# Optimization experiments

Hardware: AMD Instinct MI355X
Metric: run time of the kernel (lower is better)

The kernel has to match this reference:

```python
import jax, jax.numpy as jnp
import numpy as np

N = 50000      # nodes
E = 800000     # edges (avg degree 16)
IN = 256       # in_feats
H = 128        # hidden_feats
C = 40         # out_feats == num classes (label dim)
LPA_ITERS = 10


def setup_inputs() -> dict:
    key = jax.random.key(0)
    ks = jax.random.split(key, 9)
    features = jax.random.normal(ks[0], (N, IN), dtype=jnp.float32)
    labels = jax.random.normal(ks[1], (N, C), dtype=jnp.float32)
    mask = jax.random.randint(ks[2], (N,), 0, 2) > 0          # bool [N]
    src = jax.random.randint(ks[3], (E,), 0, N, dtype=jnp.int32)
    dst = jax.random.randint(ks[4], (E,), 0, N, dtype=jnp.int32)
    W1 = jax.random.normal(ks[5], (IN, H), dtype=jnp.float32) * (1.0 / np.sqrt(IN))
    b1 = jnp.zeros((H,), dtype=jnp.float32)
    W2 = jax.random.normal(ks[6], (H, C), dtype=jnp.float32) * (1.0 / np.sqrt(H))
    b2 = jnp.zeros((C,), dtype=jnp.float32)
    return {"features": features, "labels": labels, "mask": mask,
            "src": src, "dst": dst, "W1": W1, "b1": b1, "W2": W2, "b2": b2}


def reference(features, labels, mask, src, dst, W1, b1, W2, b2):
    ones_e = jnp.ones((E,), dtype=jnp.float32)
    deg_out = jax.ops.segment_sum(ones_e, src, num_segments=N)  # out-degree
    deg_in = jax.ops.segment_sum(ones_e, dst, num_segments=N)   # in-degree
    norm_src = jnp.maximum(deg_out, 1.0) ** -0.5                 # DGL clamps deg>=1
    norm_dst = jnp.maximum(deg_in, 1.0) ** -0.5

    def gconv(x, W, b):
        # DGL GraphConv, norm='both': D_in^{-1/2} A^T D_out^{-1/2} (x W) + b
        h = (x @ W) * norm_src[:, None]                          # [N, d_out]
        agg = jax.ops.segment_sum(h[src], dst, num_segments=N)   # gather+scatter-add
        return agg * norm_dst[:, None] + b

    x = jax.nn.relu(gconv(features, W1, b1))
    # dropout identity in eval mode
    x = gconv(x, W2, b2)

    # Label propagation: adj[src,dst]=1 so (adj @ y)[i] = sum_{(i->j)} y[j]
    masked_labels = jnp.where(mask[:, None], labels, 0.0)

    def step(y, _):
        y = jax.ops.segment_sum(y[dst], src, num_segments=N)
        y = jnp.where(mask[:, None], labels, y)
        return y, None

    y, _ = jax.lax.scan(step, masked_labels, None, length=LPA_ITERS)
    return x, y
```

## Files before the change

### kernel.cpp

```cpp
#include <hip/hip_runtime.h>

#define Nn 50000
#define Ee 800000
#define INF_ 256
#define HID 128
#define NC 40
#define CAPD 48
#define CAPS 48
#define LPA_ITERS 10
#define NB 98
#define BSH 9
#define EPB 1024
#define NBLK ((Ee + EPB - 1) / EPB)
#define G1_ROWS 64
#define G1BLK ((Nn + G1_ROWS - 1) / G1_ROWS)
#define CAPB_D 10240
#define CAPB_S 6144
#define AGG1_BLKS 2500
#define LPA_BLKS ((Nn + 31) / 32)
#define GEMM2_BLKS ((Nn + 319) / 320)
#define SCB 196

typedef __attribute__((ext_vector_type(8))) short bfrag;
typedef __attribute__((ext_vector_type(4))) float ffrag;

__device__ inline unsigned f2bf2(float a, float b) {
    unsigned ua = __float_as_uint(a); ua += 0x7FFFu + ((ua >> 16) & 1u);
    unsigned ub = __float_as_uint(b); ub += 0x7FFFu + ((ub >> 16) & 1u);
    return (ua >> 16) | (ub & 0xFFFF0000u);
}
__device__ inline unsigned short f2bf(float a) {
    unsigned ua = __float_as_uint(a); ua += 0x7FFFu + ((ua >> 16) & 1u);
    return (unsigned short)(ua >> 16);
}
__device__ inline float bf_lo(unsigned u) { return __uint_as_float(u << 16); }
__device__ inline float bf_hi(unsigned u) { return __uint_as_float(u & 0xFFFF0000u); }

__device__ inline bool read_mask(const void* mask, int node, int fmt) {
    if (fmt) return ((const unsigned char*)mask)[node] != 0;
    return ((const int*)mask)[node] != 0;
}

__global__ __launch_bounds__(256) void detect_prep(
    const unsigned int* __restrict__ m, int* flag,
    const float* __restrict__ W1, unsigned short* __restrict__ W1t) {
    int bb = blockIdx.x, tid = threadIdx.x;
    if (bb < 49) {
        int i = bb * 256 + tid;
        if (i < 12500) {
            if (m[i] > 1u) atomicOr(flag, 1);
        }
    } else {
        int c = bb - 49;
        W1t[c * INF_ + tid] = f2bf(W1[(size_t)tid * HID + c]);
    }
}

__global__ __launch_bounds__(256) void phase1(
    const int* __restrict__ src, const int* __restrict__ dst,
    const void* __restrict__ mask, const int* __restrict__ flag,
    int* __restrict__ cnt_src, int* __restrict__ cur_d, int* __restrict__ cur_s,
    unsigned* __restrict__ bkt_d, unsigned* __restrict__ bkt_s,
    const float* __restrict__ feat, const unsigned short* __restrict__ W1t,
    unsigned short* __restrict__ h1b) {
    __shared__ uint4 smem[784];
    const int tid = threadIdx.x;
    if (blockIdx.x < NBLK) {
        unsigned* stage_d = (unsigned*)smem;
        unsigned* stage_s = stage_d + EPB;
        int* hd  = (int*)(stage_s + EPB);
        int* od  = hd + NB;
        int* cd  = od + NB + 1;
        int* gd_ = cd + NB;
        int* hs  = gd_ + NB;
        int* os_ = hs + NB;
        int* cs_ = os_ + NB + 1;
        int* gs_ = cs_ + NB;
        int lane = tid & 63;
        int wid = tid >> 6;
        int e0 = blockIdx.x * EPB;
        int fmt = *flag;
        if (tid < NB) { hd[tid] = 0; hs[tid] = 0; }
        __syncthreads();

        int rs[EPB / 256], rd[EPB / 256];
        unsigned um = 0;
#pragma unroll
        for (int k = 0; k < EPB / 256; k++) {
            int e = e0 + tid + k * 256;
            rs[k] = -1; rd[k] = -1;
            if (e < Ee) {
                int s = src[e], d = dst[e];
                rs[k] = s; rd[k] = d;
                atomicAdd(&cnt_src[s], 1);
                atomicAdd(&hd[d >> BSH], 1);
                if (!read_mask(mask, s, fmt)) {
                    um |= (1u << k);
                    atomicAdd(&hs[s >> BSH], 1);
                }
            }
        }
        __syncthreads();
        if (wid < 2) {
            int* h = wid ? hs : hd;
            int* o = wid ? os_ : od;
            int i0 = lane * 2;
            int v0 = (i0 < NB) ? h[i0] : 0;
            int v1 = (i0 + 1 < NB) ? h[i0 + 1] : 0;
            int s = v0 + v1;
#pragma unroll
            for (int d = 1; d < 64; d <<= 1) {
                int t = __shfl_up(s, d);
                if (lane >= d) s += t;
            }
            int excl = s - v0 - v1;
            if (i0 < NB) o[i0] = excl;
            if (i0 + 1 < NB) o[i0 + 1] = excl + v0;
            if (lane == 63) o[NB] = s;
        }
        __syncthreads();
        if (tid < NB) {
            gd_[tid] = hd[tid] ? atomicAdd(&cur_d[tid], hd[tid]) : 0;
            gs_[tid] = hs[tid] ? atomicAdd(&cur_s[tid], hs[tid]) : 0;
            cd[tid] = od[tid];
            cs_[tid] = os_[tid];
        }
        __syncthreads();
#pragma unroll
        for (int k = 0; k < EPB / 256; k++) {
            if (rd[k] >= 0) {
                int p = atomicAdd(&cd[rd[k] >> BSH], 1);
                stage_d[p] = ((unsigned)rd[k] << 16) | (unsigned)rs[k];
                if (um & (1u << k)) {
                    int q = atomicAdd(&cs_[rs[k] >> BSH], 1);
                    stage_s[q] = ((unsigned)rs[k] << 16) | (unsigned)rd[k];
                }
            }
        }
        __syncthreads();
        for (int b = wid; b < NB; b += 4) {
            int base = od[b], cntb = hd[b], g0 = gd_[b];
            unsigned* gb = bkt_d + (size_t)b * CAPB_D;
            for (int i = lane; i < cntb; i += 64) {
                int pos = g0 + i;
                if (pos < CAPB_D) gb[pos] = stage_d[base + i];
            }
            int bs = os_[b], cnts = hs[b], gs0 = gs_[b];
            unsigned* gbs = bkt_s + (size_t)b * CAPB_S;
            for (int i = lane; i < cnts; i += 64) {
                int pos = gs0 + i;
                if (pos < CAPB_S) gbs[pos] = stage_s[bs + i];
            }
        }
    } else {
        unsigned short* lA = (unsigned short*)smem;
        unsigned short* lB = lA + G1_ROWS * 32;
        const int row0 = (blockIdx.x - NBLK) * G1_ROWS;
        const int w = tid >> 6;
        const int l = tid & 63;
        const int lane15 = l & 15;
        const int quad = l >> 4;
        const int rw0 = w * 16;

        ffrag acc[8];
#pragma unroll
        for (int t = 0; t < 8; t++) acc[t] = (ffrag){0.f, 0.f, 0.f, 0.f};

        for (int k0 = 0; k0 < INF_; k0 += 32) {
#pragma unroll
            for (int p = 0; p < 2; p++) {
                int idx = tid + p * 256;
                int r = idx >> 3, c4 = idx & 7;
                int grow = row0 + r;
                float4 v = make_float4(0.f, 0.f, 0.f, 0.f);
                if (grow < Nn)
                    v = *(const float4*)(feat + (size_t)grow * INF_ + k0 + c4 * 4);
                uint2 pk;
                pk.x = f2bf2(v.x, v.y);
                pk.y = f2bf2(v.z, v.w);
                *(uint2*)((char*)lA + r * 64 + c4 * 8) = pk;
            }
#pragma unroll
            for (int p = 0; p < 2; p++) {
                int idx = tid + p * 256;
                int col = idx >> 2, q = idx & 3;
                uint4 v = *(const uint4*)((const char*)W1t + col * 512 + k0 * 2 + q * 16);
                *(uint4*)((char*)lB + col * 64 + q * 16) = v;
            }
            __syncthreads();
            int arow = rw0 + lane15;
            bfrag af = *(const bfrag*)((const char*)lA + arow * 64 + quad * 16);
#pragma unroll
            for (int t = 0; t < 8; t++) {
                int col = t * 16 + lane15;
                bfrag bf = *(const bfrag*)((const char*)lB + col * 64 + quad * 16);
                acc[t] = __builtin_amdgcn_mfma_f32_16x16x32_bf16(af, bf, acc[t], 0, 0, 0);
            }
            __syncthreads();
        }
#pragma unroll
        for (int t = 0; t < 8; t++) {
#pragma unroll
            for (int i = 0; i < 4; i++) {
                int grow = row0 + rw0 + quad * 4 + i;
                if (grow < Nn)
                    h1b[(size_t)grow * HID + t * 16 + lane15] = f2bf(acc[t][i]);
            }
        }
    }
}

__global__ __launch_bounds__(256) void build_csr_both(
    const unsigned* __restrict__ bkt_d, const int* __restrict__ cur_d,
    const unsigned* __restrict__ bkt_s, const int* __restrict__ cur_s,
    const void* __restrict__ mask, const int* __restrict__ flag,
    const int* __restrict__ cnt_src,
    int* __restrict__ adj_dst, int* __restrict__ cnt_dst,
    int* __restrict__ adj_s, int* __restrict__ cnt_u, int* __restrict__ cnt_m,
    int* __restrict__ n_un, int* __restrict__ ulist,
    unsigned short* __restrict__ h1b) {
    __shared__ int lu[512], lm[512];
    int bb = blockIdx.x, tid = threadIdx.x;
    lu[tid] = 0; lu[tid + 256] = 0; lm[tid] = 0; lm[tid + 256] = 0;
    __syncthreads();
    if (bb < NB) {
        int b = bb;
        int n = cur_d[b]; if (n > CAPB_D) n = CAPB_D;
        int n0 = b << BSH;
        const unsigned* base = bkt_d + (size_t)b * CAPB_D;
        for (int i = tid; i < n; i += 256) {
            unsigned r = base[i];
            int d = r >> 16, s = r & 0xffff;
            int sl = atomicAdd(&lu[d - n0], 1);
            if (sl < CAPD) adj_dst[d * CAPD + sl] = s;
        }
        __syncthreads();
        int g0 = n0 + tid;
        if (g0 < Nn) cnt_dst[g0] = lu[tid];
        g0 += 256;
        if (g0 < Nn) cnt_dst[g0] = lu[tid + 256];
    } else if (bb < 2 * NB) {
        int b = bb - NB;
        int fmt = *flag;
        int n = cur_s[b]; if (n > CAPB_S) n = CAPB_S;
        int n0 = b << BSH;
        const unsigned* base = bkt_s + (size_t)b * CAPB_S;
        for (int i = tid; i < n; i += 256) {
            unsigned r = base[i];
            int s = r >> 16, d = r & 0xffff;
            if (read_mask(mask, d, fmt)) {
                int sl = atomicAdd(&lm[s - n0], 1);
                if (sl < CAPS) adj_s[s * CAPS + (CAPS - 1 - sl)] = d;
            } else {
                int sl = atomicAdd(&lu[s - n0], 1);
                if (sl < CAPS) adj_s[s * CAPS + sl] = d;
            }
        }
        __syncthreads();
        int g0 = n0 + tid;
        if (g0 < Nn) {
            cnt_u[g0] = lu[tid]; cnt_m[g0] = lm[tid];
            if (!read_mask(mask, g0, fmt)) {
                int p = atomicAdd(n_un, 1);
                ulist[p] = g0;
            }
        }
        g0 += 256;
        if (g0 < Nn) {
            cnt_u[g0] = lu[tid + 256]; cnt_m[g0] = lm[tid + 256];
            if (!read_mask(mask, g0, fmt)) {
                int p = atomicAdd(n_un, 1);
                ulist[p] = g0;
            }
        }
    } else {
        int b = bb - 2 * NB;
        int rbase = b * 256;
        int c8 = tid & 7;
#pragma unroll 1
        for (int it = 0; it < 8; it++) {
            int r = rbase + it * 32 + (tid >> 3);
            if (r >= Nn) continue;
            int cs = cnt_src[r];
            float nr = rsqrtf((float)(cs > 1 ? cs : 1));
            uint4* row = (uint4*)(h1b + (size_t)r * HID);
#pragma unroll
            for (int h = 0; h < 2; h++) {
                uint4 u = row[c8 * 2 + h];
                u.x = f2bf2(bf_lo(u.x) * nr, bf_hi(u.x) * nr);
                u.y = f2bf2(bf_lo(u.y) * nr, bf_hi(u.y) * nr);
                u.z = f2bf2(bf_lo(u.z) * nr, bf_hi(u.z) * nr);
                u.w = f2bf2(bf_lo(u.w) * nr, bf_hi(u.w) * nr);
                row[c8 * 2 + h] = u;
            }
        }
    }
}


__device__ inline void do_lpa_const(
    int g, int l, const float4* __restrict__ labels,
    const int* __restrict__ ulist, const int* __restrict__ adj_s,
    const int* __restrict__ cnt_m, float4* __restrict__ sconst,
    uint2* __restrict__ y1b) {
    int u = ulist[g];
    int cm = cnt_m[u];
    int cnt = cm < CAPS ? cm : CAPS;
    const int* lst = adj_s + (size_t)u * CAPS + (CAPS - cnt);
    float4 s = make_float4(0.f, 0.f, 0.f, 0.f);
    int e = 0;
    for (; e + 8 <= cnt; e += 8) {
        float4 v[8];
#pragma unroll
        for (int q = 0; q < 8; q++) v[q] = labels[(size_t)lst[e + q] * 10 + l];
#pragma unroll
        for (int q = 0; q < 8; q++) {
            s.x += v[q].x; s.y += v[q].y; s.z += v[q].z; s.w += v[q].w;
        }
    }
    for (; e + 4 <= cnt; e += 4) {
        float4 v[4];
#pragma unroll
        for (int q = 0; q < 4; q++) v[q] = labels[(size_t)lst[e + q] * 10 + l];
#pragma unroll
        for (int q = 0; q < 4; q++) {
            s.x += v[q].x; s.y += v[q].y; s.z += v[q].z; s.w += v[q].w;
        }
    }
    for (; e < cnt; e++) {
        float4 a = labels[(size_t)lst[e] * 10 + l];
        s.x += a.x; s.y += a.y; s.z += a.z; s.w += a.w;
    }
    sconst[(size_t)u * 10 + l] = s;
    uint2 pk; pk.x = f2bf2(s.x, s.y); pk.y = f2bf2(s.z, s.w);
    y1b[(size_t)u * 10 + l] = pk;
}

__device__ inline void do_lpa_mid(
    int g, int l, const uint2* __restrict__ ycur,
    const int* __restrict__ ulist, const int* __restrict__ adj_s,
    const int* __restrict__ cnt_u, const float4* __restrict__ sconst,
    uint2* __restrict__ ynext) {
    int u = ulist[g];
    int cu = cnt_u[u];
    int cnt = cu < CAPS ? cu : CAPS;
    const int* lst = adj_s + (size_t)u * CAPS;
    float4 s = sconst[(size_t)u * 10 + l];
    int e = 0;
    for (; e + 8 <= cnt; e += 8) {
        uint2 v[8];
#pragma unroll
        for (int q = 0; q < 8; q++) v[q] = ycur[(size_t)lst[e + q] * 10 + l];
#pragma unroll
        for (int q = 0; q < 8; q++) {
            s.x += bf_lo(v[q].x); s.y += bf_hi(v[q].x);
            s.z += bf_lo(v[q].y); s.w += bf_hi(v[q].y);
        }
    }
    for (; e + 4 <= cnt; e += 4) {
        uint2 v[4];
#pragma unroll
        for (int q = 0; q < 4; q++) v[q] = ycur[(size_t)lst[e + q] * 10 + l];
#pragma unroll
        for (int q = 0; q < 4; q++) {
            s.x += bf_lo(v[q].x); s.y += bf_hi(v[q].x);
            s.z += bf_lo(v[q].y); s.w += bf_hi(v[q].y);
        }
    }
    for (; e < cnt; e++) {
        uint2 v = ycur[(size_t)lst[e] * 10 + l];
        s.x += bf_lo(v.x); s.y += bf_hi(v.x);
        s.z += bf_lo(v.y); s.w += bf_hi(v.y);
    }
    uint2 pk; pk.x = f2bf2(s.x, s.y); pk.y = f2bf2(s.z, s.w);
    ynext[(size_t)u * 10 + l] = pk;
}

__device__ inline void do_agg2(
    int node, int l, const uint2* __restrict__ h2b,
    const int* __restrict__ adj_dst, const int* __restrict__ cnt_dst,
    const float4* __restrict__ b2, float4* __restrict__ out_x) {
    int dg = cnt_dst[node];
    int cnt = dg < CAPD ? dg : CAPD;
    const int* lst = adj_dst + (size_t)node * CAPD;
    float s0 = 0.f, s1 = 0.f, s2 = 0.f, s3 = 0.f;
    int e = 0;
    for (; e + 8 <= cnt; e += 8) {
        uint2 u[8];
#pragma unroll
        for (int q = 0; q < 8; q++) u[q] = h2b[(size_t)lst[e + q] * 10 + l];
#pragma unroll
        for (int q = 0; q < 8; q++) {
            s0 += bf_lo(u[q].x); s1 += bf_hi(u[q].x);
            s2 += bf_lo(u[q].y); s3 += bf_hi(u[q].y);
        }
    }
    for (; e + 4 <= cnt; e += 4) {
        uint2 u[4];
#pragma unroll
        for (int q = 0; q < 4; q++) u[q] = h2b[(size_t)lst[e + q] * 10 + l];
#pragma unroll
        for (int q = 0; q < 4; q++) {
            s0 += bf_lo(u[q].x); s1 += bf_hi(u[q].x);
            s2 += bf_lo(u[q].y); s3 += bf_hi(u[q].y);
        }
    }
    for (; e < cnt; e++) {
        uint2 u = h2b[(size_t)lst[e] * 10 + l];
        s0 += bf_lo(u.x); s1 += bf_hi(u.x);
        s2 += bf_lo(u.y); s3 += bf_hi(u.y);
    }
    float nrm = rsqrtf((float)(dg > 1 ? dg : 1));
    float4 bb = b2[l];
    float4 v;
    v.x = s0 * nrm + bb.x;
    v.y = s1 * nrm + bb.y;
    v.z = s2 * nrm + bb.z;
    v.w = s3 * nrm + bb.w;
    out_x[(size_t)node * 10 + l] = v;
}

__global__ __launch_bounds__(320) void k_agg1_lconst(
    const uint4* __restrict__ h1b, const int* __restrict__ adj_dst,
    const int* __restrict__ cnt_dst, const float4* __restrict__ b1,
    uint4* __restrict__ x1b,
    const float4* __restrict__ labels, const void* __restrict__ mask,
    const int* __restrict__ flag, const int* __restrict__ n_un,
    const int* __restrict__ ulist, const int* __restrict__ adj_s,
    const int* __restrict__ cnt_m, float4* __restrict__ sconst,
    uint2* __restrict__ y1b, float4* __restrict__ out_y4) {
    int bb = blockIdx.x, tid = threadIdx.x;
    if (bb < AGG1_BLKS) {
        const int node = bb * 20 + (tid >> 4);
        const int l = tid & 15;
        int dg = cnt_dst[node];
        int cnt = dg < CAPD ? dg : CAPD;
        const int* lst = adj_dst + (size_t)node * CAPD;
        float s0 = 0.f, s1 = 0.f, s2 = 0.f, s3 = 0.f;
        float s4 = 0.f, s5 = 0.f, s6 = 0.f, s7 = 0.f;
        int e = 0;
        for (; e + 8 <= cnt; e += 8) {
            uint4 u[8];
#pragma unroll
            for (int q = 0; q < 8; q++) u[q] = h1b[(size_t)lst[e + q] * 16 + l];
#pragma unroll
            for (int q = 0; q < 8; q++) {
                s0 += bf_lo(u[q].x); s1 += bf_hi(u[q].x);
                s2 += bf_lo(u[q].y); s3 += bf_hi(u[q].y);
                s4 += bf_lo(u[q].z); s5 += bf_hi(u[q].z);
                s6 += bf_lo(u[q].w); s7 += bf_hi(u[q].w);
            }
        }
        for (; e < cnt; e++) {
            uint4 u = h1b[(size_t)lst[e] * 16 + l];
            s0 += bf_lo(u.x); s1 += bf_hi(u.x);
            s2 += bf_lo(u.y); s3 += bf_hi(u.y);
            s4 += bf_lo(u.z); s5 += bf_hi(u.z);
            s6 += bf_lo(u.w); s7 += bf_hi(u.w);
        }
        float nrm = rsqrtf((float)(dg > 1 ? dg : 1));
        float4 bb0 = b1[l * 2], bb1 = b1[l * 2 + 1];
        float v0x = fmaxf(s0 * nrm + bb0.x, 0.f);
        float v0y = fmaxf(s1 * nrm + bb0.y, 0.f);
        float v0z = fmaxf(s2 * nrm + bb0.z, 0.f);
        float v0w = fmaxf(s3 * nrm + bb0.w, 0.f);
        float v1x = fmaxf(s4 * nrm + bb1.x, 0.f);
        float v1y = fmaxf(s5 * nrm + bb1.y, 0.f);
        float v1z = fmaxf(s6 * nrm + bb1.z, 0.f);
        float v1w = fmaxf(s7 * nrm + bb1.w, 0.f);
        uint4 pk4;
        pk4.x = f2bf2(v0x, v0y);
        pk4.y = f2bf2(v0z, v0w);
        pk4.z = f2bf2(v1x, v1y);
        pk4.w = f2bf2(v1z, v1w);
        x1b[(size_t)node * 16 + l] = pk4;
    } else {
        int lb = bb - AGG1_BLKS;
        int fmt = *flag;
        int i = lb * 320 + tid;
        if (i < Nn * 10) {
            int node = i / 10;
            if (read_mask(mask, node, fmt)) out_y4[i] = labels[i];
        }
        int g = lb * 32 + tid / 10;
        if (g < *n_un)
            do_lpa_const(g, tid % 10, labels, ulist, adj_s, cnt_m, sconst, y1b);
    }
}

__global__ __launch_bounds__(320) void k_gemm2_mid(
    const uint4* __restrict__ x1b, const float4* __restrict__ W2,
    const int* __restrict__ cnt_src, unsigned* __restrict__ h2b,
    const uint2* __restrict__ ycur, const int* __restrict__ n_un,
    const int* __restrict__ ulist, const int* __restrict__ adj_s,
    const int* __restrict__ cnt_u, const float4* __restrict__ sconst,
    uint2* __restrict__ ynext) {
    __shared__ float lw[HID * NC];
    int bb = blockIdx.x, tid = threadIdx.x;
    if (bb < GEMM2_BLKS) {
        for (int i = tid; i < HID * NC / 4; i += 320)
            ((float4*)lw)[i] = W2[i];
        __syncthreads();
        int r = bb * 320 + tid;
        if (r >= Nn) return;
        const uint4* xr = x1b + (size_t)r * 16;
        float4 acc[10];
#pragma unroll
        for (int j = 0; j < 10; j++) acc[j] = make_float4(0.f, 0.f, 0.f, 0.f);
        for (int kk = 0; kk < 16; kk++) {
            uint4 u = xr[kk];
            float xv[8];
            xv[0] = bf_lo(u.x); xv[1] = bf_hi(u.x);
            xv[2] = bf_lo(u.y); xv[3] = bf_hi(u.y);
            xv[4] = bf_lo(u.z); xv[5] = bf_hi(u.z);
            xv[6] = bf_lo(u.w); xv[7] = bf_hi(u.w);
#pragma unroll
            for (int s = 0; s < 8; s++) {
                float x = xv[s];
                const float4* wrow = (const float4*)(lw + (kk * 8 + s) * NC);
#pragma unroll
                for (int j = 0; j < 10; j++) {
                    float4 w = wrow[j];
                    acc[j].x += x * w.x; acc[j].y += x * w.y;
                    acc[j].z += x * w.z; acc[j].w += x * w.w;
                }
            }
        }
        int dg = cnt_src[r];
        float nrm = rsqrtf((float)(dg > 1 ? dg : 1));
        uint2* out = (uint2*)(h2b + (size_t)r * 20);
#pragma unroll
        for (int j = 0; j < 10; j++) {
            uint2 pk;
            pk.x = f2bf2(acc[j].x * nrm, acc[j].y * nrm);
            pk.y = f2bf2(acc[j].z * nrm, acc[j].w * nrm);
            out[j] = pk;
        }
    } else {
        int g = (bb - GEMM2_BLKS) * 32 + tid / 10;
        if (g < *n_un)
            do_lpa_mid(g, tid % 10, ycur, ulist, adj_s, cnt_u, sconst, ynext);
    }
}

__global__ __launch_bounds__(320) void k_agg2_mid(
    const uint2* __restrict__ h2b, const int* __restrict__ adj_dst,
    const int* __restrict__ cnt_dst, const float4* __restrict__ b2,
    float4* __restrict__ out_x,
    const uint2* __restrict__ ycur, const int* __restrict__ n_un,
    const int* __restrict__ ulist, const int* __restrict__ adj_s,
    const int* __restrict__ cnt_u, const float4* __restrict__ sconst,
    uint2* __restrict__ ynext) {
    int bb = blockIdx.x, tid = threadIdx.x;
    if (bb < LPA_BLKS) {
        int node = bb * 32 + tid / 10;
        if (node < Nn)
            do_agg2(node, tid % 10, h2b, adj_dst, cnt_dst, b2, out_x);
    } else {
        int g = (bb - LPA_BLKS) * 32 + tid / 10;
        if (g < *n_un)
            do_lpa_mid(g, tid % 10, ycur, ulist, adj_s, cnt_u, sconst, ynext);
    }
}

__global__ __launch_bounds__(320) void lpa_mid(
    const uint2* __restrict__ ycur, const int* __restrict__ n_un,
    const int* __restrict__ ulist, const int* __restrict__ adj_s,
    const int* __restrict__ cnt_u, const float4* __restrict__ sconst,
    uint2* __restrict__ ynext) {
    int g = blockIdx.x * 32 + threadIdx.x / 10;
    if (g < *n_un)
        do_lpa_mid(g, threadIdx.x % 10, ycur, ulist, adj_s, cnt_u, sconst, ynext);
}

__global__ __launch_bounds__(320) void lpa_last(
    const uint2* __restrict__ ycur, const int* __restrict__ n_un,
    const int* __restrict__ ulist, const int* __restrict__ adj_s,
    const int* __restrict__ cnt_u, const float4* __restrict__ sconst,
    float4* __restrict__ out_y) {
    int g = blockIdx.x * 32 + threadIdx.x / 10;
    int l = threadIdx.x % 10;
    if (g >= *n_un) return;
    int u = ulist[g];
    int cu = cnt_u[u];
    int cnt = cu < CAPS ? cu : CAPS;
    const int* lst = adj_s + (size_t)u * CAPS;
    float4 s = sconst[(size_t)u * 10 + l];
    int e = 0;
    for (; e + 8 <= cnt; e += 8) {
        uint2 v[8];
#pragma unroll
        for (int q = 0; q < 8; q++) v[q] = ycur[(size_t)lst[e + q] * 10 + l];
#pragma unroll
        for (int q = 0; q < 8; q++) {
            s.x += bf_lo(v[q].x); s.y += bf_hi(v[q].x);
            s.z += bf_lo(v[q].y); s.w += bf_hi(v[q].y);
        }
    }
    for (; e + 4 <= cnt; e += 4) {
        uint2 v[4];
#pragma unroll
        for (int q = 0; q < 4; q++) v[q] = ycur[(size_t)lst[e + q] * 10 + l];
#pragma unroll
        for (int q = 0; q < 4; q++) {
            s.x += bf_lo(v[q].x); s.y += bf_hi(v[q].x);
            s.z += bf_lo(v[q].y); s.w += bf_hi(v[q].y);
        }
    }
    for (; e < cnt; e++) {
        uint2 v = ycur[(size_t)lst[e] * 10 + l];
        s.x += bf_lo(v.x); s.y += bf_hi(v.x);
        s.z += bf_lo(v.y); s.w += bf_hi(v.y);
    }
    out_y[(size_t)u * 10 + l] = s;
}

extern "C" void kernel_launch(void* const* d_in, const int* in_sizes, int n_in,
                              void* d_out, int out_size, void* d_ws, size_t ws_size,
                              hipStream_t stream) {
    const float* feat   = (const float*)d_in[0];
    const float* labels = (const float*)d_in[1];
    const void*  mask   = d_in[2];
    const int*   src    = (const int*)d_in[3];
    const int*   dst    = (const int*)d_in[4];
    const float* W1     = (const float*)d_in[5];
    const float* b1     = (const float*)d_in[6];
    const float* W2     = (const float*)d_in[7];
    const float* b2     = (const float*)d_in[8];

    float* out_x = (float*)d_out;
    float* out_y = out_x + (size_t)Nn * NC;

    char* ws = (char*)d_ws;
    size_t off = 0;
    auto alloc = [&](size_t bytes) -> void* {
        void* p = ws + off;
        off += (bytes + 255) & ~(size_t)255;
        return p;
    };
    int* flag    = (int*)alloc(256);
    int* n_un    = flag + 1;
    int* cnt_src = (int*)alloc((size_t)Nn * 4);
    int* cur_d   = (int*)alloc(512);
    int* cur_s   = (int*)alloc(512);
    size_t zero_bytes = off;
    int* cnt_dst = (int*)alloc((size_t)Nn * 4);
    int* cnt_u   = (int*)alloc((size_t)Nn * 4);
    int* cnt_m   = (int*)alloc((size_t)Nn * 4);
    int* ulist   = (int*)alloc((size_t)Nn * 4);
    unsigned short* W1t = (unsigned short*)alloc((size_t)HID * INF_ * 2);
    unsigned* bkt_d = (unsigned*)alloc((size_t)NB * CAPB_D * 4);
    unsigned* bkt_s = (unsigned*)alloc((size_t)NB * CAPB_S * 4);
    unsigned short* h1b = (unsigned short*)alloc((size_t)Nn * HID * 2);
    uint4* x1b = (uint4*)alloc((size_t)Nn * HID * 2);
    int* adj_s   = (int*)alloc((size_t)Nn * CAPS * 4);
    int* adj_dst = (int*)alloc((size_t)Nn * CAPD * 4);
    unsigned* h2b = (unsigned*)alloc((size_t)Nn * NC * 2);
    float* sconst = (float*)alloc((size_t)Nn * NC * 4);
    uint2* y1b = (uint2*)alloc((size_t)Nn * NC * 2);
    uint2* y2b = (uint2*)alloc((size_t)Nn * NC * 2);

    hipMemsetAsync(d_ws, 0, zero_bytes, stream);

    detect_prep<<<49 + HID, 256, 0, stream>>>((const unsigned int*)mask, flag,
                                              W1, W1t);
    phase1<<<NBLK + G1BLK, 256, 0, stream>>>(
        src, dst, mask, flag, cnt_src, cur_d, cur_s, bkt_d, bkt_s,
        feat, W1t, h1b);
    build_csr_both<<<NB * 2 + SCB, 256, 0, stream>>>(
        bkt_d, cur_d, bkt_s, cur_s, mask, flag, cnt_src,
        adj_dst, cnt_dst, adj_s, cnt_u, cnt_m, n_un, ulist, h1b);

    k_agg1_lconst<<<AGG1_BLKS + LPA_BLKS, 320, 0, stream>>>(
        (const uint4*)h1b, adj_dst, cnt_dst, (const float4*)b1, x1b,
        (const float4*)labels, mask, flag, n_un, ulist, adj_s,
        cnt_m, (float4*)sconst, y1b, (float4*)out_y);
    k_gemm2_mid<<<GEMM2_BLKS + LPA_BLKS, 320, 0, stream>>>(
        (const uint4*)x1b, (const float4*)W2, cnt_src, h2b,
        y1b, n_un, ulist, adj_s, cnt_u, (const float4*)sconst, y2b);
    k_agg2_mid<<<LPA_BLKS + LPA_BLKS, 320, 0, stream>>>(
        (const uint2*)h2b, adj_dst, cnt_dst, (const float4*)b2, (float4*)out_x,
        y2b, n_un, ulist, adj_s, cnt_u, (const float4*)sconst, y1b);

    const uint2* cur = y1b;
    for (int i = 0; i < 6; i++) {
        uint2* nxt = (i & 1) ? y1b : y2b;
        lpa_mid<<<LPA_BLKS, 320, 0, stream>>>(
            cur, n_un, ulist, adj_s, cnt_u, (const float4*)sconst, nxt);
        cur = nxt;
    }
    lpa_last<<<LPA_BLKS, 320, 0, stream>>>(
        cur, n_un, ulist, adj_s, cnt_u, (const float4*)sconst, (float4*)out_y);
}
```

Measured before the change: 362.7 us.

## Split GCN stages into chunks co-scheduled with more label-propagation iterations

Result: slower. 396.7 us (+9.4%).

```diff
diff --git a/kernel.cpp b/kernel.cpp
--- a/kernel.cpp
+++ b/kernel.cpp
@@ -16,10 +16,15 @@
 #define G1BLK ((Nn + G1_ROWS - 1) / G1_ROWS)
 #define CAPB_D 10240
 #define CAPB_S 6144
-#define AGG1_BLKS 2500
 #define LPA_BLKS ((Nn + 31) / 32)
-#define GEMM2_BLKS ((Nn + 319) / 320)
 #define SCB 196
+#define A1T1 834
+#define A1T2 833
+#define A1T3 833
+#define G2H1 79
+#define G2H2 78
+#define AG2H1 782
+#define AG2H2 781
 
 typedef __attribute__((ext_vector_type(8))) short bfrag;
 typedef __attribute__((ext_vector_type(4))) float ffrag;
@@ -298,6 +303,53 @@
 }
 
 
+__device__ inline void do_agg1b(
+    int node, int l, const uint4* __restrict__ h1b,
+    const int* __restrict__ adj_dst, const int* __restrict__ cnt_dst,
+    const float4* __restrict__ b1, uint4* __restrict__ x1b) {
+    int dg = cnt_dst[node];
+    int cnt = dg < CAPD ? dg : CAPD;
+    const int* lst = adj_dst + (size_t)node * CAPD;
+    float s0 = 0.f, s1 = 0.f, s2 = 0.f, s3 = 0.f;
+    float s4 = 0.f, s5 = 0.f, s6 = 0.f, s7 = 0.f;
+    int e = 0;
+    for (; e + 8 <= cnt; e += 8) {
+        uint4 u[8];
+#pragma unroll
+        for (int q = 0; q < 8; q++) u[q] = h1b[(size_t)lst[e + q] * 16 + l];
+#pragma unroll
+        for (int q = 0; q < 8; q++) {
+            s0 += bf_lo(u[q].x); s1 += bf_hi(u[q].x);
+            s2 += bf_lo(u[q].y); s3 += bf_hi(u[q].y);
+            s4 += bf_lo(u[q].z); s5 += bf_hi(u[q].z);
+            s6 += bf_lo(u[q].w); s7 += bf_hi(u[q].w);
+        }
+    }
+    for (; e < cnt; e++) {
+        uint4 u = h1b[(size_t)lst[e] * 16 + l];
+        s0 += bf_lo(u.x); s1 += bf_hi(u.x);
+        s2 += bf_lo(u.y); s3 += bf_hi(u.y);
+        s4 += bf_lo(u.z); s5 += bf_hi(u.z);
+        s6 += bf_lo(u.w); s7 += bf_hi(u.w);
+    }
+    float nrm = rsqrtf((float)(dg > 1 ? dg : 1));
+    float4 bb0 = b1[l * 2], bb1 = b1[l * 2 + 1];
+    float v0x = fmaxf(s0 * nrm + bb0.x, 0.f);
+    float v0y = fmaxf(s1 * nrm + bb0.y, 0.f);
+    float v0z = fmaxf(s2 * nrm + bb0.z, 0.f);
+    float v0w = fmaxf(s3 * nrm + bb0.w, 0.f);
+    float v1x = fmaxf(s4 * nrm + bb1.x, 0.f);
+    float v1y = fmaxf(s5 * nrm + bb1.y, 0.f);
+    float v1z = fmaxf(s6 * nrm + bb1.z, 0.f);
+    float v1w = fmaxf(s7 * nrm + bb1.w, 0.f);
+    uint4 pk4;
+    pk4.x = f2bf2(v0x, v0y);
+    pk4.y = f2bf2(v0z, v0w);
+    pk4.z = f2bf2(v1x, v1y);
+    pk4.w = f2bf2(v1z, v1w);
+    x1b[(size_t)node * 16 + l] = pk4;
+}
+
 __device__ inline void do_lpa_const(
     int g, int l, const float4* __restrict__ labels,
     const int* __restrict__ ulist, const int* __restrict__ adj_s,
@@ -420,7 +472,9 @@
     out_x[(size_t)node * 10 + l] = v;
 }
 
+
 __global__ __launch_bounds__(320) void k_agg1_lconst(
+    const int node0, const int nagg,
     const uint4* __restrict__ h1b, const int* __restrict__ adj_dst,
     const int* __restrict__ cnt_dst, const float4* __restrict__ b1,
     uint4* __restrict__ x1b,
@@ -430,52 +484,11 @@
     const int* __restrict__ cnt_m, float4* __restrict__ sconst,
     uint2* __restrict__ y1b, float4* __restrict__ out_y4) {
     int bb = blockIdx.x, tid = threadIdx.x;
-    if (bb < AGG1_BLKS) {
-        const int node = bb * 20 + (tid >> 4);
-        const int l = tid & 15;
-        int dg = cnt_dst[node];
-        int cnt = dg < CAPD ? dg : CAPD;
-        const int* lst = adj_dst + (size_t)node * CAPD;
-        float s0 = 0.f, s1 = 0.f, s2 = 0.f, s3 = 0.f;
-        float s4 = 0.f, s5 = 0.f, s6 = 0.f, s7 = 0.f;
-        int e = 0;
-        for (; e + 8 <= cnt; e += 8) {
-            uint4 u[8];
-#pragma unroll
-            for (int q = 0; q < 8; q++) u[q] = h1b[(size_t)lst[e + q] * 16 + l];
-#pragma unroll
-            for (int q = 0; q < 8; q++) {
-                s0 += bf_lo(u[q].x); s1 += bf_hi(u[q].x);
-                s2 += bf_lo(u[q].y); s3 += bf_hi(u[q].y);
-                s4 += bf_lo(u[q].z); s5 += bf_hi(u[q].z);
-                s6 += bf_lo(u[q].w); s7 += bf_hi(u[q].w);
-            }
-        }
-        for (; e < cnt; e++) {
-            uint4 u = h1b[(size_t)lst[e] * 16 + l];
-            s0 += bf_lo(u.x); s1 += bf_hi(u.x);
-            s2 += bf_lo(u.y); s3 += bf_hi(u.y);
-            s4 += bf_lo(u.z); s5 += bf_hi(u.z);
-            s6 += bf_lo(u.w); s7 += bf_hi(u.w);
-        }
-        float nrm = rsqrtf((float)(dg > 1 ? dg : 1));
-        float4 bb0 = b1[l * 2], bb1 = b1[l * 2 + 1];
-        float v0x = fmaxf(s0 * nrm + bb0.x, 0.f);
-        float v0y = fmaxf(s1 * nrm + bb0.y, 0.f);
-        float v0z = fmaxf(s2 * nrm + bb0.z, 0.f);
-        float v0w = fmaxf(s3 * nrm + bb0.w, 0.f);
-        float v1x = fmaxf(s4 * nrm + bb1.x, 0.f);
-        float v1y = fmaxf(s5 * nrm + bb1.y, 0.f);
-        float v1z = fmaxf(s6 * nrm + bb1.z, 0.f);
-        float v1w = fmaxf(s7 * nrm + bb1.w, 0.f);
-        uint4 pk4;
-        pk4.x = f2bf2(v0x, v0y);
-        pk4.y = f2bf2(v0z, v0w);
-        pk4.z = f2bf2(v1x, v1y);
-        pk4.w = f2bf2(v1z, v1w);
-        x1b[(size_t)node * 16 + l] = pk4;
+    if (bb < nagg) {
+        do_agg1b(node0 + bb * 20 + (tid >> 4), tid & 15,
+                 h1b, adj_dst, cnt_dst, b1, x1b);
     } else {
-        int lb = bb - AGG1_BLKS;
+        int lb = bb - nagg;
         int fmt = *flag;
         int i = lb * 320 + tid;
         if (i < Nn * 10) {
@@ -488,7 +501,28 @@
     }
 }
 
+__global__ __launch_bounds__(320) void k_agg1_mid(
+    const int node0, const int nagg,
+    const uint4* __restrict__ h1b, const int* __restrict__ adj_dst,
+    const int* __restrict__ cnt_dst, const float4* __restrict__ b1,
+    uint4* __restrict__ x1b,
+    const uint2* __restrict__ ycur, const int* __restrict__ n_un,
+    const int* __restrict__ ulist, const int* __restrict__ adj_s,
+    const int* __restrict__ cnt_u, const float4* __restrict__ sconst,
+    uint2* __restrict__ ynext) {
+    int bb = blockIdx.x, tid = threadIdx.x;
+    if (bb < nagg) {
+        do_agg1b(node0 + bb * 20 + (tid >> 4), tid & 15,
+                 h1b, adj_dst, cnt_dst, b1, x1b);
+    } else {
+        int g = (bb - nagg) * 32 + tid / 10;
+        if (g < *n_un)
+            do_lpa_mid(g, tid % 10, ycur, ulist, adj_s, cnt_u, sconst, ynext);
+    }
+}
+
 __global__ __launch_bounds__(320) void k_gemm2_mid(
+    const int row0, const int ngem,
     const uint4* __restrict__ x1b, const float4* __restrict__ W2,
     const int* __restrict__ cnt_src, unsigned* __restrict__ h2b,
     const uint2* __restrict__ ycur, const int* __restrict__ n_un,
@@ -497,11 +531,11 @@
     uint2* __restrict__ ynext) {
     __shared__ float lw[HID * NC];
     int bb = blockIdx.x, tid = threadIdx.x;
-    if (bb < GEMM2_BLKS) {
+    if (bb < ngem) {
         for (int i = tid; i < HID * NC / 4; i += 320)
             ((float4*)lw)[i] = W2[i];
         __syncthreads();
-        int r = bb * 320 + tid;
+        int r = row0 + bb * 320 + tid;
         if (r >= Nn) return;
         const uint4* xr = x1b + (size_t)r * 16;
         float4 acc[10];
@@ -537,13 +571,14 @@
             out[j] = pk;
         }
     } else {
-        int g = (bb - GEMM2_BLKS) * 32 + tid / 10;
+        int g = (bb - ngem) * 32 + tid / 10;
         if (g < *n_un)
             do_lpa_mid(g, tid % 10, ycur, ulist, adj_s, cnt_u, sconst, ynext);
     }
 }
 
 __global__ __launch_bounds__(320) void k_agg2_mid(
+    const int node0, const int nagg,
     const uint2* __restrict__ h2b, const int* __restrict__ adj_dst,
     const int* __restrict__ cnt_dst, const float4* __restrict__ b2,
     float4* __restrict__ out_x,
@@ -552,12 +587,12 @@
     const int* __restrict__ cnt_u, const float4* __restrict__ sconst,
     uint2* __restrict__ ynext) {
     int bb = blockIdx.x, tid = threadIdx.x;
-    if (bb < LPA_BLKS) {
-        int node = bb * 32 + tid / 10;
+    if (bb < nagg) {
+        int node = node0 + bb * 32 + tid / 10;
         if (node < Nn)
             do_agg2(node, tid % 10, h2b, adj_dst, cnt_dst, b2, out_x);
     } else {
-        int g = (bb - LPA_BLKS) * 32 + tid / 10;
+        int g = (bb - nagg) * 32 + tid / 10;
         if (g < *n_un)
             do_lpa_mid(g, tid % 10, ycur, ulist, adj_s, cnt_u, sconst, ynext);
     }
@@ -671,24 +706,35 @@
         bkt_d, cur_d, bkt_s, cur_s, mask, flag, cnt_src,
         adj_dst, cnt_dst, adj_s, cnt_u, cnt_m, n_un, ulist, h1b);
 
-    k_agg1_lconst<<<AGG1_BLKS + LPA_BLKS, 320, 0, stream>>>(
-        (const uint4*)h1b, adj_dst, cnt_dst, (const float4*)b1, x1b,
+    k_agg1_lconst<<<A1T1 + LPA_BLKS, 320, 0, stream>>>(
+        0, A1T1, (const uint4*)h1b, adj_dst, cnt_dst, (const float4*)b1, x1b,
         (const float4*)labels, mask, flag, n_un, ulist, adj_s,
         cnt_m, (float4*)sconst, y1b, (float4*)out_y);
-    k_gemm2_mid<<<GEMM2_BLKS + LPA_BLKS, 320, 0, stream>>>(
-        (const uint4*)x1b, (const float4*)W2, cnt_src, h2b,
+    k_agg1_mid<<<A1T2 + LPA_BLKS, 320, 0, stream>>>(
+        16680, A1T2, (const uint4*)h1b, adj_dst, cnt_dst, (const float4*)b1,
+        x1b, y1b, n_un, ulist, adj_s, cnt_u, (const float4*)sconst, y2b);
+    k_agg1_mid<<<A1T3 + LPA_BLKS, 320, 0, stream>>>(
+        33340, A1T3, (const uint4*)h1b, adj_dst, cnt_dst, (const float4*)b1,
+        x1b, y2b, n_un, ulist, adj_s, cnt_u, (const float4*)sconst, y1b);
+    k_gemm2_mid<<<G2H1 + LPA_BLKS, 320, 0, stream>>>(
+        0, G2H1, (const uint4*)x1b, (const float4*)W2, cnt_src, h2b,
         y1b, n_un, ulist, adj_s, cnt_u, (const float4*)sconst, y2b);
-    k_agg2_mid<<<LPA_BLKS + LPA_BLKS, 320, 0, stream>>>(
-        (const uint2*)h2b, adj_dst, cnt_dst, (const float4*)b2, (float4*)out_x,
+    k_gemm2_mid<<<G2H2 + LPA_BLKS, 320, 0, stream>>>(
+        25280, G2H2, (const uint4*)x1b, (const float4*)W2, cnt_src, h2b,
         y2b, n_un, ulist, adj_s, cnt_u, (const float4*)sconst, y1b);
-
-    const uint2* cur = y1b;
-    for (int i = 0; i < 6; i++) {
-        uint2* nxt = (i & 1) ? y1b : y2b;
-        lpa_mid<<<LPA_BLKS, 320, 0, stream>>>(
-            cur, n_un, ulist, adj_s, cnt_u, (const float4*)sconst, nxt);
-        cur = nxt;
-    }
+    k_agg2_mid<<<AG2H1 + LPA_BLKS, 320, 0, stream>>>(
+        0, AG2H1, (const uint2*)h2b, adj_dst, cnt_dst, (const float4*)b2,
+        (float4*)out_x, y1b, n_un, ulist, adj_s, cnt_u,
+        (const float4*)sconst, y2b);
+    k_agg2_mid<<<AG2H2 + LPA_BLKS, 320, 0, stream>>>(
+        25024, AG2H2, (const uint2*)h2b, adj_dst, cnt_dst, (const float4*)b2,
+        (float4*)out_x, y2b, n_un, ulist, adj_s, cnt_u,
+        (const float4*)sconst, y1b);
+
+    lpa_mid<<<LPA_BLKS, 320, 0, stream>>>(
+        y1b, n_un, ulist, adj_s, cnt_u, (const float4*)sconst, y2b);
+    lpa_mid<<<LPA_BLKS, 320, 0, stream>>>(
+        y2b, n_un, ulist, adj_s, cnt_u, (const float4*)sconst, y1b);
     lpa_last<<<LPA_BLKS, 320, 0, stream>>>(
-        cur, n_un, ulist, adj_s, cnt_u, (const float4*)sconst, (float4*)out_y);
-}
+        y1b, n_un, ulist, adj_s, cnt_u, (const float4*)sconst, (float4*)out_y);
+}
```
